# Kernel optimization log

Hardware: AMD Instinct MI355X
Metric: run time of the kernel (lower is better)

## Reference

```python
import jax, jax.numpy as jnp
import numpy as np

N_ENT = 40000      # n_ent_vocab
NUM_POS = 24       # n_rel_vocab // 2
N_REL = 48         # n_rel_vocab (fwd + inverse relations)
BODY_LEN = 3
N_EDGES = 300000
BATCH = 64
THR = 1e-20


def setup_inputs() -> dict:
    key = jax.random.key(0)
    ks = jax.random.split(key, 8)
    return {
        "q_head": jax.random.randint(ks[0], (BATCH,), 0, N_ENT, dtype=jnp.int32),
        "q_rel": jax.random.randint(ks[1], (BATCH,), 0, NUM_POS, dtype=jnp.int32),
        "t": jax.random.randint(ks[2], (BATCH,), 0, N_ENT, dtype=jnp.int32),
        # dec_output is a softmax over relations -> positive weights in (0,1)
        "attention": jax.random.uniform(ks[3], (BATCH, BODY_LEN, N_REL), dtype=jnp.float32),
        "edge_head": jax.random.randint(ks[4], (N_EDGES,), 0, N_ENT, dtype=jnp.int32),
        "edge_tail": jax.random.randint(ks[5], (N_EDGES,), 0, N_ENT, dtype=jnp.int32),
        "edge_rel": jax.random.randint(ks[6], (N_EDGES,), 0, NUM_POS, dtype=jnp.int32),
        # uncertain-KG confidence values stored in the sparse adjacency
        "edge_val": jax.random.uniform(ks[7], (N_EDGES,), dtype=jnp.float32),
    }


def reference(q_head, q_rel, t, attention, edge_head, edge_tail, edge_rel, edge_val):
    """Fused equivalent of Translator.forwardAllNLP.

    database[r] are sparse [N_ENT, N_ENT] matrices; here the whole multigraph is
    one edge list (edge_head, edge_tail, edge_rel, edge_val). torch.sparse.mm
    per relation + attention-weighted accumulation becomes a single gather /
    segment_sum pass over all relations at once.
    """
    B = q_head.shape[0]
    # zero out the query triples in the (shared) database, as in the torch code
    killed = ((edge_head[None, :] == q_head[:, None])
              & (edge_tail[None, :] == t[:, None])
              & (edge_rel[None, :] == q_rel[:, None])).any(axis=0)
    vals = jnp.where(killed, 0.0, edge_val)  # [E]

    mem = jax.nn.one_hot(q_head, N_ENT, dtype=jnp.float32)  # [B, N_ENT]
    for step in range(BODY_LEN):
        attn = attention[:, step]                 # [B, N_REL]
        a_fwd = attn[:, edge_rel]                 # [B, E]  attention[:,step,r]
        a_rev = attn[:, edge_rel + NUM_POS]       # [B, E]  attention[:,step,r+num_pos]
        gh = mem[:, edge_head] * vals             # [B, E]  sparse.mm(mem, A_r)
        gt = mem[:, edge_tail] * vals             # [B, E]  sparse.mm(mem, A_r^T)
        fwd_msg = jax.ops.segment_sum((gh * a_fwd).T, edge_tail, num_segments=N_ENT).T
        rev_msg = jax.ops.segment_sum((gt * a_rev).T, edge_head, num_segments=N_ENT).T
        # self-loop term: memories * attention[:, step, -1]
        mem = fwd_msg + rev_msg + mem * attn[:, -1:]

    mem = mem / jnp.maximum(THR, mem.sum(axis=1, keepdims=True))
    # -sum(one_hot(t) * log(max(thr, mem))) == -log(max(thr, mem[b, t[b]]))
    tgt_prob = mem[jnp.arange(B), t]
    batch_loss = -jnp.log(jnp.maximum(THR, tgt_prob)).mean()
    return batch_loss, mem
```

## Files before the change

kernel.cpp:

```cpp
#include <hip/hip_runtime.h>
#include <hip/hip_bf16.h>

#define N_ENT 40000
#define NB 64
#define BODY_LEN 3
#define N_REL 48
#define NUM_POS 24
#define THR 1e-20f


__global__ void k_vals(const int* __restrict__ qh, const int* __restrict__ qr,
                       const int* __restrict__ tt, const int* __restrict__ eh,
                       const int* __restrict__ et, const int* __restrict__ er,
                       const float* __restrict__ ev, float* __restrict__ vals,
                       float* __restrict__ sums, int nE) {
    __shared__ long long s_key[NB];
    int tid = threadIdx.x;
    if (tid < NB) {
        s_key[tid] = ((long long)qh[tid] << 32) | ((long long)tt[tid] << 8) | (long long)qr[tid];
        if (blockIdx.x == 0) sums[tid] = 0.0f;
    }
    __syncthreads();
    int i = blockIdx.x * blockDim.x + tid;
    if (i < nE) {
        long long k = ((long long)eh[i] << 32) | ((long long)et[i] << 8) | (long long)er[i];
        bool killed = false;
#pragma unroll
        for (int b = 0; b < NB; ++b) killed |= (s_key[b] == k);
        vals[i] = killed ? 0.0f : ev[i];
    }
}

__global__ void k_init_decay(const int* __restrict__ qh, const float* __restrict__ attn,
                             float* __restrict__ nxt) {
    __shared__ float s_d[NB];
    __shared__ int s_q[NB];
    if (threadIdx.x < NB) {
        s_d[threadIdx.x] = attn[threadIdx.x * (BODY_LEN * N_REL) + 0 * N_REL + (N_REL - 1)];
        s_q[threadIdx.x] = qh[threadIdx.x];
    }
    __syncthreads();
    int i4 = blockIdx.x * 256 + threadIdx.x;
    int ent = (i4 * 4) >> 6;
    int b0 = (i4 * 4) & 63;
    float4 w;
    w.x = (s_q[b0 + 0] == ent) ? s_d[b0 + 0] : 0.0f;
    w.y = (s_q[b0 + 1] == ent) ? s_d[b0 + 1] : 0.0f;
    w.z = (s_q[b0 + 2] == ent) ? s_d[b0 + 2] : 0.0f;
    w.w = (s_q[b0 + 3] == ent) ? s_d[b0 + 3] : 0.0f;
    ((float4*)nxt)[i4] = w;
}

__global__ void k_decay(const float* __restrict__ oldm, float* __restrict__ nxt,
                        const float* __restrict__ attn, int step,
                        unsigned char* __restrict__ active) {
    __shared__ float s_d[NB];
    if (threadIdx.x < NB)
        s_d[threadIdx.x] = attn[threadIdx.x * (BODY_LEN * N_REL) + step * N_REL + (N_REL - 1)];
    __syncthreads();
    int i4 = blockIdx.x * 256 + threadIdx.x;
    float4 v = ((const float4*)oldm)[i4];
    int b0 = (threadIdx.x * 4) & 63;
    float4 w;
    w.x = v.x * s_d[b0 + 0];
    w.y = v.y * s_d[b0 + 1];
    w.z = v.z * s_d[b0 + 2];
    w.w = v.w * s_d[b0 + 3];
    ((float4*)nxt)[i4] = w;
    bool nz = (v.x != 0.0f) | (v.y != 0.0f) | (v.z != 0.0f) | (v.w != 0.0f);
    unsigned long long m = __ballot(nz);
    int lane = threadIdx.x & 63;
    if ((lane & 15) == 0) {
        int ent = (i4 * 4) >> 6;
        active[ent] = ((m >> lane) & 0xFFFFULL) ? 1 : 0;
    }
}

template <bool STEP0>
__global__ __launch_bounds__(256) void k_step(
    const int* __restrict__ eh, const int* __restrict__ et, const int* __restrict__ er,
    const float* __restrict__ vals, const float* __restrict__ attn, int step,
    const float* __restrict__ oldm, const unsigned char* __restrict__ active,
    const int* __restrict__ qh, float* __restrict__ nxt, int nE) {
    __shared__ float s_attn[NB][N_REL + 1];
    int tid = threadIdx.x;
    for (int idx = tid; idx < NB * N_REL; idx += 256) {
        int b = idx / N_REL, r = idx % N_REL;
        s_attn[b][r] = attn[b * (BODY_LEN * N_REL) + step * N_REL + r];
    }
    __syncthreads();
    int lane = tid & 63;
    int myqh = STEP0 ? qh[lane] : 0;
    int wave = (blockIdx.x * 256 + tid) >> 6;
    int nW = (gridDim.x * 256) >> 6;

    int e = wave;
    for (; e + nW < nE; e += 2 * nW) {
        int e1 = e + nW;
        int h0 = eh[e],  t0 = et[e],  r0 = er[e];  float v0 = vals[e];
        int h1 = eh[e1], t1 = et[e1], r1 = er[e1]; float v1 = vals[e1];
        if (STEP0) {
            bool hh0 = (h0 == myqh), ht0 = (t0 == myqh);
            bool hh1 = (h1 == myqh), ht1 = (t1 == myqh);
            unsigned long long b0m = __ballot(hh0 || ht0);
            unsigned long long b1m = __ballot(hh1 || ht1);
            if (b0m && v0 != 0.0f) {
                float c1 = (hh0 ? v0 : 0.0f) * s_attn[lane][r0];
                float c2 = (ht0 ? v0 : 0.0f) * s_attn[lane][r0 + NUM_POS];
                if (c1 != 0.0f) atomicAdd(&nxt[(size_t)t0 * 64 + lane], c1);
                if (c2 != 0.0f) atomicAdd(&nxt[(size_t)h0 * 64 + lane], c2);
            }
            if (b1m && v1 != 0.0f) {
                float c1 = (hh1 ? v1 : 0.0f) * s_attn[lane][r1];
                float c2 = (ht1 ? v1 : 0.0f) * s_attn[lane][r1 + NUM_POS];
                if (c1 != 0.0f) atomicAdd(&nxt[(size_t)t1 * 64 + lane], c1);
                if (c2 != 0.0f) atomicAdd(&nxt[(size_t)h1 * 64 + lane], c2);
            }
        } else {
            unsigned a0 = (unsigned)active[h0] | (unsigned)active[t0];
            unsigned a1 = (unsigned)active[h1] | (unsigned)active[t1];
            if (a0 && v0 != 0.0f) {
                float mh = oldm[(size_t)h0 * 64 + lane];
                float mt = oldm[(size_t)t0 * 64 + lane];
                float c1 = mh * v0 * s_attn[lane][r0];
                float c2 = mt * v0 * s_attn[lane][r0 + NUM_POS];
                if (c1 != 0.0f) atomicAdd(&nxt[(size_t)t0 * 64 + lane], c1);
                if (c2 != 0.0f) atomicAdd(&nxt[(size_t)h0 * 64 + lane], c2);
            }
            if (a1 && v1 != 0.0f) {
                float mh = oldm[(size_t)h1 * 64 + lane];
                float mt = oldm[(size_t)t1 * 64 + lane];
                float c1 = mh * v1 * s_attn[lane][r1];
                float c2 = mt * v1 * s_attn[lane][r1 + NUM_POS];
                if (c1 != 0.0f) atomicAdd(&nxt[(size_t)t1 * 64 + lane], c1);
                if (c2 != 0.0f) atomicAdd(&nxt[(size_t)h1 * 64 + lane], c2);
            }
        }
    }
    for (; e < nE; e += nW) {
        int h = eh[e], t = et[e], r = er[e];
        float v = vals[e];
        if (STEP0) {
            bool hh = (h == myqh), ht = (t == myqh);
            if (__ballot(hh || ht) == 0ULL || v == 0.0f) continue;
            float c1 = (hh ? v : 0.0f) * s_attn[lane][r];
            float c2 = (ht ? v : 0.0f) * s_attn[lane][r + NUM_POS];
            if (c1 != 0.0f) atomicAdd(&nxt[(size_t)t * 64 + lane], c1);
            if (c2 != 0.0f) atomicAdd(&nxt[(size_t)h * 64 + lane], c2);
        } else {
            if (((unsigned)active[h] | (unsigned)active[t]) == 0 || v == 0.0f) continue;
            float mh = oldm[(size_t)h * 64 + lane];
            float mt = oldm[(size_t)t * 64 + lane];
            float c1 = mh * v * s_attn[lane][r];
            float c2 = mt * v * s_attn[lane][r + NUM_POS];
            if (c1 != 0.0f) atomicAdd(&nxt[(size_t)t * 64 + lane], c1);
            if (c2 != 0.0f) atomicAdd(&nxt[(size_t)h * 64 + lane], c2);
        }
    }
}

__global__ void k_sums(const float* __restrict__ mem, float* __restrict__ sums) {
    __shared__ float s_s[NB];
    if (threadIdx.x < NB) s_s[threadIdx.x] = 0.0f;
    __syncthreads();
    const float4* m4 = (const float4*)mem;
    const int total4 = NB * N_ENT / 4;
    float4 acc = {0.0f, 0.0f, 0.0f, 0.0f};
    for (int i = blockIdx.x * 256 + threadIdx.x; i < total4; i += gridDim.x * 256) {
        float4 v = m4[i];
        acc.x += v.x; acc.y += v.y; acc.z += v.z; acc.w += v.w;
    }
    int b0 = (threadIdx.x * 4) & 63;
    atomicAdd(&s_s[b0 + 0], acc.x);
    atomicAdd(&s_s[b0 + 1], acc.y);
    atomicAdd(&s_s[b0 + 2], acc.z);
    atomicAdd(&s_s[b0 + 3], acc.w);
    __syncthreads();
    if (threadIdx.x < NB) atomicAdd(&sums[threadIdx.x], s_s[threadIdx.x]);
}

__global__ void k_norm_tr(const float* __restrict__ mem, const float* __restrict__ sums,
                          const int* __restrict__ tt, float* __restrict__ out) {
    if (blockIdx.x == N_ENT / 64) {
        int b = threadIdx.x;
        if (b < 64) {
            float p = mem[(size_t)tt[b] * 64 + b] / fmaxf(THR, sums[b]);
            float l = -logf(fmaxf(THR, p));
#pragma unroll
            for (int off = 32; off > 0; off >>= 1) l += __shfl_down(l, off);
            if (b == 0) out[0] = l * (1.0f / 64.0f);
        }
        return;
    }
    __shared__ float tile[64][65];
    __shared__ float s_inv[64];
    int tid = threadIdx.x;
    int e0 = blockIdx.x * 64;
    if (tid < 64) s_inv[tid] = 1.0f / fmaxf(THR, sums[tid]);
    const float4* m4 = (const float4*)(mem + (size_t)e0 * 64);
#pragma unroll
    for (int k = 0; k < 4; ++k) {
        int i4 = k * 256 + tid;
        float4 v = m4[i4];
        int el = i4 >> 4, b0 = (i4 * 4) & 63;
        tile[el][b0 + 0] = v.x; tile[el][b0 + 1] = v.y;
        tile[el][b0 + 2] = v.z; tile[el][b0 + 3] = v.w;
    }
    __syncthreads();
#pragma unroll
    for (int k = 0; k < 16; ++k) {
        int idx = k * 256 + tid;
        int el = idx & 63, b = idx >> 6;
        out[1 + (size_t)b * N_ENT + e0 + el] = tile[el][b] * s_inv[b];
    }
}

extern "C" void kernel_launch(void* const* d_in, const int* in_sizes, int n_in,
                              void* d_out, int out_size, void* d_ws, size_t ws_size,
                              hipStream_t stream) {
    const int*   qh   = (const int*)d_in[0];
    const int*   qr   = (const int*)d_in[1];
    const int*   tt   = (const int*)d_in[2];
    const float* attn = (const float*)d_in[3];
    const int*   eh   = (const int*)d_in[4];
    const int*   et   = (const int*)d_in[5];
    const int*   er   = (const int*)d_in[6];
    const float* ev   = (const float*)d_in[7];
    float* out = (float*)d_out;
    int nE = in_sizes[4];

    const size_t MEM_BYTES = (size_t)NB * N_ENT * sizeof(float);
    char* ws = (char*)d_ws;
    float*         vals   = (float*)ws;
    float*         sums   = (float*)(ws + (2u << 20));
    unsigned char* active = (unsigned char*)(ws + (2u << 20) + 4096);
    float* memA = (float*)(ws + (4u << 20));
    float* memB;
    size_t needBoth = (size_t)(4u << 20) + 2 * MEM_BYTES;
    if (ws_size >= needBoth)
        memB = (float*)(ws + (4u << 20) + MEM_BYTES);
    else
        memB = out + 1;

    const int NE_F4 = NB * N_ENT / 4 / 256;

    k_vals<<<(nE + 255) / 256, 256, 0, stream>>>(qh, qr, tt, eh, et, er, ev, vals, sums, nE);

    k_init_decay<<<NE_F4, 256, 0, stream>>>(qh, attn, memA);
    k_step<true><<<2048, 256, 0, stream>>>(eh, et, er, vals, attn, 0,
                                           nullptr, nullptr, qh, memA, nE);
    float* cur = memA;
    float* nxt = memB;
    for (int s = 1; s < BODY_LEN; ++s) {
        k_decay<<<NE_F4, 256, 0, stream>>>(cur, nxt, attn, s, active);
        k_step<false><<<2048, 256, 0, stream>>>(eh, et, er, vals, attn, s,
                                                cur, active, nullptr, nxt, nE);
        float* tmp = cur; cur = nxt; nxt = tmp;
    }

    k_sums<<<128, 256, 0, stream>>>(cur, sums);
    k_norm_tr<<<N_ENT / 64 + 1, 256, 0, stream>>>(cur, sums, tt, out);
}
```

Before: 183.5 us.

## Build per-call CSR adjacency and propagate only over frontier entities

Replaces the full edge-list sweep per step with a CSR adjacency built each call (degree count, scan, scatter with the query-triple kill folded in) and a frontier list of entities with nonzero memory. Each step kernel then walks only the neighbour lists of active entities, broadcasting edge metadata across the wave with shuffles. This removes reading all edges per step and the active-byte checks. It adds four build kernels, including a single-block scan, plus random atomic scatter into the CSR.

```diff
diff --git a/kernel.cpp b/kernel.cpp
--- a/kernel.cpp
+++ b/kernel.cpp
@@ -9,30 +9,94 @@
 #define THR 1e-20f
 
 
-__global__ void k_vals(const int* __restrict__ qh, const int* __restrict__ qr,
-                       const int* __restrict__ tt, const int* __restrict__ eh,
-                       const int* __restrict__ et, const int* __restrict__ er,
-                       const float* __restrict__ ev, float* __restrict__ vals,
-                       float* __restrict__ sums, int nE) {
+__global__ void k_zero(int* __restrict__ deg, int* __restrict__ fcnt,
+                       float* __restrict__ sums) {
+    int i = blockIdx.x * 256 + threadIdx.x;
+    if (i < N_ENT) deg[i] = 0;
+    if (i < 3) fcnt[i] = 0;
+    if (i >= 64 && i < 128) sums[i - 64] = 0.0f;
+}
+
+__global__ void k_count(const int* __restrict__ eh, const int* __restrict__ et,
+                        int* __restrict__ deg, int nE) {
+    int i = blockIdx.x * 256 + threadIdx.x;
+    if (i < nE) {
+        atomicAdd(&deg[eh[i]], 1);
+        atomicAdd(&deg[et[i]], 1);
+    }
+}
+
+__global__ void k_scan(const int* __restrict__ deg, int* __restrict__ offs,
+                       int* __restrict__ csrCur) {
+    __shared__ int s_part[1024];
+    int t = threadIdx.x;
+    int base = t * 40;
+    int end = min(N_ENT, base + 40);
+    int local = 0;
+    for (int i = base; i < end; ++i) local += deg[i];
+    s_part[t] = local;
+    __syncthreads();
+    for (int off = 1; off < 1024; off <<= 1) {
+        int add = (t >= off) ? s_part[t - off] : 0;
+        __syncthreads();
+        s_part[t] += add;
+        __syncthreads();
+    }
+    int run = (t == 0) ? 0 : s_part[t - 1];
+    for (int i = base; i < end; ++i) {
+        int d = deg[i];
+        offs[i] = run;
+        csrCur[i] = run;
+        run += d;
+    }
+    if (t == 1023) offs[N_ENT] = s_part[1023];
+}
+
+__global__ void k_scatter(const int* __restrict__ qh, const int* __restrict__ qr,
+                          const int* __restrict__ tt, const int* __restrict__ eh,
+                          const int* __restrict__ et, const int* __restrict__ er,
+                          const float* __restrict__ ev, int* __restrict__ csrCur,
+                          uint2* __restrict__ csr, int nE) {
     __shared__ long long s_key[NB];
     int tid = threadIdx.x;
-    if (tid < NB) {
+    if (tid < NB)
         s_key[tid] = ((long long)qh[tid] << 32) | ((long long)tt[tid] << 8) | (long long)qr[tid];
-        if (blockIdx.x == 0) sums[tid] = 0.0f;
-    }
-    __syncthreads();
-    int i = blockIdx.x * blockDim.x + tid;
+    __syncthreads();
+    int i = blockIdx.x * 256 + tid;
     if (i < nE) {
-        long long k = ((long long)eh[i] << 32) | ((long long)et[i] << 8) | (long long)er[i];
+        int h = eh[i], t = et[i], r = er[i];
+        long long k = ((long long)h << 32) | ((long long)t << 8) | (long long)r;
         bool killed = false;
 #pragma unroll
         for (int b = 0; b < NB; ++b) killed |= (s_key[b] == k);
-        vals[i] = killed ? 0.0f : ev[i];
+        float v = killed ? 0.0f : ev[i];
+        unsigned vb = __float_as_uint(v);
+        int sh = atomicAdd(&csrCur[h], 1);
+        csr[sh] = make_uint2((unsigned)t | ((unsigned)r << 16), vb);
+        int st = atomicAdd(&csrCur[t], 1);
+        csr[st] = make_uint2((unsigned)h | ((unsigned)(r + NUM_POS) << 16), vb);
+    }
+}
+
+__device__ __forceinline__ void frontier_append(unsigned long long m, int lane,
+                                                int ent, int* fcnt, int* flist) {
+    bool flag = ((lane & 15) == 0) && ((m >> lane) & 0xFFFFULL);
+    unsigned long long am = __ballot(flag);
+    if (am) {
+        int leader = __ffsll((long long)am) - 1;
+        int basef = 0;
+        if (lane == leader) basef = atomicAdd(fcnt, __popcll(am));
+        basef = __shfl(basef, leader);
+        if (flag) {
+            int rank = __popcll(am & ((1ULL << lane) - 1ULL));
+            flist[basef + rank] = ent;
+        }
     }
 }
 
 __global__ void k_init_decay(const int* __restrict__ qh, const float* __restrict__ attn,
-                             float* __restrict__ nxt) {
+                             float* __restrict__ nxt, int* __restrict__ fcnt,
+                             int* __restrict__ flist) {
     __shared__ float s_d[NB];
     __shared__ int s_q[NB];
     if (threadIdx.x < NB) {
@@ -44,16 +108,21 @@
     int ent = (i4 * 4) >> 6;
     int b0 = (i4 * 4) & 63;
     float4 w;
+    bool nz = false;
     w.x = (s_q[b0 + 0] == ent) ? s_d[b0 + 0] : 0.0f;
     w.y = (s_q[b0 + 1] == ent) ? s_d[b0 + 1] : 0.0f;
     w.z = (s_q[b0 + 2] == ent) ? s_d[b0 + 2] : 0.0f;
     w.w = (s_q[b0 + 3] == ent) ? s_d[b0 + 3] : 0.0f;
+    nz = (s_q[b0 + 0] == ent) | (s_q[b0 + 1] == ent) |
+         (s_q[b0 + 2] == ent) | (s_q[b0 + 3] == ent);
     ((float4*)nxt)[i4] = w;
+    unsigned long long m = __ballot(nz);
+    frontier_append(m, threadIdx.x & 63, ent, fcnt, flist);
 }
 
 __global__ void k_decay(const float* __restrict__ oldm, float* __restrict__ nxt,
                         const float* __restrict__ attn, int step,
-                        unsigned char* __restrict__ active) {
+                        int* __restrict__ fcnt, int* __restrict__ flist) {
     __shared__ float s_d[NB];
     if (threadIdx.x < NB)
         s_d[threadIdx.x] = attn[threadIdx.x * (BODY_LEN * N_REL) + step * N_REL + (N_REL - 1)];
@@ -69,19 +138,17 @@
     ((float4*)nxt)[i4] = w;
     bool nz = (v.x != 0.0f) | (v.y != 0.0f) | (v.z != 0.0f) | (v.w != 0.0f);
     unsigned long long m = __ballot(nz);
-    int lane = threadIdx.x & 63;
-    if ((lane & 15) == 0) {
-        int ent = (i4 * 4) >> 6;
-        active[ent] = ((m >> lane) & 0xFFFFULL) ? 1 : 0;
-    }
+    int ent = (i4 * 4) >> 6;
+    frontier_append(m, threadIdx.x & 63, ent, fcnt, flist);
 }
 
 template <bool STEP0>
-__global__ __launch_bounds__(256) void k_step(
-    const int* __restrict__ eh, const int* __restrict__ et, const int* __restrict__ er,
-    const float* __restrict__ vals, const float* __restrict__ attn, int step,
-    const float* __restrict__ oldm, const unsigned char* __restrict__ active,
-    const int* __restrict__ qh, float* __restrict__ nxt, int nE) {
+__global__ __launch_bounds__(256) void k_fstep(
+    const uint2* __restrict__ csr, const int* __restrict__ offs,
+    const int* __restrict__ flist, const int* __restrict__ fcnt,
+    const float* __restrict__ attn, int step,
+    const float* __restrict__ oldm, const int* __restrict__ qh,
+    float* __restrict__ nxt) {
     __shared__ float s_attn[NB][N_REL + 1];
     int tid = threadIdx.x;
     for (int idx = tid; idx < NB * N_REL; idx += 256) {
@@ -91,70 +158,27 @@
     __syncthreads();
     int lane = tid & 63;
     int myqh = STEP0 ? qh[lane] : 0;
-    int wave = (blockIdx.x * 256 + tid) >> 6;
+    int n = *fcnt;
+    int w = (blockIdx.x * 256 + tid) >> 6;
     int nW = (gridDim.x * 256) >> 6;
-
-    int e = wave;
-    for (; e + nW < nE; e += 2 * nW) {
-        int e1 = e + nW;
-        int h0 = eh[e],  t0 = et[e],  r0 = er[e];  float v0 = vals[e];
-        int h1 = eh[e1], t1 = et[e1], r1 = er[e1]; float v1 = vals[e1];
-        if (STEP0) {
-            bool hh0 = (h0 == myqh), ht0 = (t0 == myqh);
-            bool hh1 = (h1 == myqh), ht1 = (t1 == myqh);
-            unsigned long long b0m = __ballot(hh0 || ht0);
-            unsigned long long b1m = __ballot(hh1 || ht1);
-            if (b0m && v0 != 0.0f) {
-                float c1 = (hh0 ? v0 : 0.0f) * s_attn[lane][r0];
-                float c2 = (ht0 ? v0 : 0.0f) * s_attn[lane][r0 + NUM_POS];
-                if (c1 != 0.0f) atomicAdd(&nxt[(size_t)t0 * 64 + lane], c1);
-                if (c2 != 0.0f) atomicAdd(&nxt[(size_t)h0 * 64 + lane], c2);
+    for (int f = w; f < n; f += nW) {
+        int e = flist[f];
+        float src = STEP0 ? ((myqh == e) ? 1.0f : 0.0f)
+                          : oldm[(size_t)e * 64 + lane];
+        int base = offs[e];
+        int cnt = offs[e + 1] - base;
+        for (int k0 = 0; k0 < cnt; k0 += 64) {
+            uint2 slot = make_uint2(0u, 0u);
+            if (k0 + lane < cnt) slot = csr[base + k0 + lane];
+            int lim = min(64, cnt - k0);
+            for (int j = 0; j < lim; ++j) {
+                unsigned meta = (unsigned)__shfl((int)slot.x, j);
+                float v = __uint_as_float((unsigned)__shfl((int)slot.y, j));
+                if (v == 0.0f) continue;
+                float val = src * v * s_attn[lane][meta >> 16];
+                if (val != 0.0f)
+                    atomicAdd(&nxt[(size_t)(meta & 0xFFFFu) * 64 + lane], val);
             }
-            if (b1m && v1 != 0.0f) {
-                float c1 = (hh1 ? v1 : 0.0f) * s_attn[lane][r1];
-                float c2 = (ht1 ? v1 : 0.0f) * s_attn[lane][r1 + NUM_POS];
-                if (c1 != 0.0f) atomicAdd(&nxt[(size_t)t1 * 64 + lane], c1);
-                if (c2 != 0.0f) atomicAdd(&nxt[(size_t)h1 * 64 + lane], c2);
-            }
-        } else {
-            unsigned a0 = (unsigned)active[h0] | (unsigned)active[t0];
-            unsigned a1 = (unsigned)active[h1] | (unsigned)active[t1];
-            if (a0 && v0 != 0.0f) {
-                float mh = oldm[(size_t)h0 * 64 + lane];
-                float mt = oldm[(size_t)t0 * 64 + lane];
-                float c1 = mh * v0 * s_attn[lane][r0];
-                float c2 = mt * v0 * s_attn[lane][r0 + NUM_POS];
-                if (c1 != 0.0f) atomicAdd(&nxt[(size_t)t0 * 64 + lane], c1);
-                if (c2 != 0.0f) atomicAdd(&nxt[(size_t)h0 * 64 + lane], c2);
-            }
-            if (a1 && v1 != 0.0f) {
-                float mh = oldm[(size_t)h1 * 64 + lane];
-                float mt = oldm[(size_t)t1 * 64 + lane];
-                float c1 = mh * v1 * s_attn[lane][r1];
-                float c2 = mt * v1 * s_attn[lane][r1 + NUM_POS];
-                if (c1 != 0.0f) atomicAdd(&nxt[(size_t)t1 * 64 + lane], c1);
-                if (c2 != 0.0f) atomicAdd(&nxt[(size_t)h1 * 64 + lane], c2);
-            }
-        }
-    }
-    for (; e < nE; e += nW) {
-        int h = eh[e], t = et[e], r = er[e];
-        float v = vals[e];
-        if (STEP0) {
-            bool hh = (h == myqh), ht = (t == myqh);
-            if (__ballot(hh || ht) == 0ULL || v == 0.0f) continue;
-            float c1 = (hh ? v : 0.0f) * s_attn[lane][r];
-            float c2 = (ht ? v : 0.0f) * s_attn[lane][r + NUM_POS];
-            if (c1 != 0.0f) atomicAdd(&nxt[(size_t)t * 64 + lane], c1);
-            if (c2 != 0.0f) atomicAdd(&nxt[(size_t)h * 64 + lane], c2);
-        } else {
-            if (((unsigned)active[h] | (unsigned)active[t]) == 0 || v == 0.0f) continue;
-            float mh = oldm[(size_t)h * 64 + lane];
-            float mt = oldm[(size_t)t * 64 + lane];
-            float c1 = mh * v * s_attn[lane][r];
-            float c2 = mt * v * s_attn[lane][r + NUM_POS];
-            if (c1 != 0.0f) atomicAdd(&nxt[(size_t)t * 64 + lane], c1);
-            if (c2 != 0.0f) atomicAdd(&nxt[(size_t)h * 64 + lane], c2);
         }
     }
 }
@@ -231,33 +255,46 @@
 
     const size_t MEM_BYTES = (size_t)NB * N_ENT * sizeof(float);
     char* ws = (char*)d_ws;
-    float*         vals   = (float*)ws;
-    float*         sums   = (float*)(ws + (2u << 20));
-    unsigned char* active = (unsigned char*)(ws + (2u << 20) + 4096);
-    float* memA = (float*)(ws + (4u << 20));
+    int*   offs   = (int*)ws;
+    int*   deg    = (int*)(ws + (192u << 10));
+    int*   csrCur = (int*)(ws + (384u << 10));
+    int*   flist  = (int*)(ws + (576u << 10));
+    int*   fcnt   = (int*)(ws + (768u << 10));
+    float* sums   = (float*)(ws + (768u << 10) + 256);
+    float* memA   = (float*)(ws + (1u << 20));
     float* memB;
-    size_t needBoth = (size_t)(4u << 20) + 2 * MEM_BYTES;
-    if (ws_size >= needBoth)
-        memB = (float*)(ws + (4u << 20) + MEM_BYTES);
-    else
+    char*  csrBase;
+    size_t csrBytes = (size_t)2 * nE * sizeof(uint2);
+    size_t needBoth = (size_t)(1u << 20) + 2 * MEM_BYTES + csrBytes;
+    if (ws_size >= needBoth) {
+        memB = (float*)(ws + (1u << 20) + MEM_BYTES);
+        csrBase = ws + (1u << 20) + 2 * MEM_BYTES;
+    } else {
         memB = out + 1;
+        csrBase = ws + (1u << 20) + MEM_BYTES;
+    }
+    uint2* csr = (uint2*)csrBase;
 
     const int NE_F4 = NB * N_ENT / 4 / 256;
-
-    k_vals<<<(nE + 255) / 256, 256, 0, stream>>>(qh, qr, tt, eh, et, er, ev, vals, sums, nE);
-
-    k_init_decay<<<NE_F4, 256, 0, stream>>>(qh, attn, memA);
-    k_step<true><<<2048, 256, 0, stream>>>(eh, et, er, vals, attn, 0,
-                                           nullptr, nullptr, qh, memA, nE);
-    float* cur = memA;
-    float* nxt = memB;
+    const int EB = (nE + 255) / 256;
+
+    k_zero<<<(N_ENT + 255) / 256, 256, 0, stream>>>(deg, fcnt, sums);
+    k_count<<<EB, 256, 0, stream>>>(eh, et, deg, nE);
+    k_scan<<<1, 1024, 0, stream>>>(deg, offs, csrCur);
+    k_scatter<<<EB, 256, 0, stream>>>(qh, qr, tt, eh, et, er, ev, csrCur, csr, nE);
+
+    k_init_decay<<<NE_F4, 256, 0, stream>>>(qh, attn, memA, fcnt + 0, flist);
+    k_fstep<true><<<16, 256, 0, stream>>>(csr, offs, flist, fcnt + 0, attn, 0,
+                                          nullptr, qh, memA);
+    float* curm = memA;
+    float* nxtm = memB;
     for (int s = 1; s < BODY_LEN; ++s) {
-        k_decay<<<NE_F4, 256, 0, stream>>>(cur, nxt, attn, s, active);
-        k_step<false><<<2048, 256, 0, stream>>>(eh, et, er, vals, attn, s,
-                                                cur, active, nullptr, nxt, nE);
-        float* tmp = cur; cur = nxt; nxt = tmp;
-    }
-
-    k_sums<<<128, 256, 0, stream>>>(cur, sums);
-    k_norm_tr<<<N_ENT / 64 + 1, 256, 0, stream>>>(cur, sums, tt, out);
-}
+        k_decay<<<NE_F4, 256, 0, stream>>>(curm, nxtm, attn, s, fcnt + s, flist);
+        k_fstep<false><<<1024, 256, 0, stream>>>(csr, offs, flist, fcnt + s, attn, s,
+                                                 curm, nullptr, nxtm);
+        float* tmp = curm; curm = nxtm; nxtm = tmp;
+    }
+
+    k_sums<<<128, 256, 0, stream>>>(curm, sums);
+    k_norm_tr<<<N_ENT / 64 + 1, 256, 0, stream>>>(curm, sums, tt, out);
+}
```

Measured after the change: 394.6 us. 2.15x slower.
